# Kernel optimization log

Measured on AMD Instinct MI355X. Metric: run time of the kernel, lower is better.

## Reference

```python
import jax, jax.numpy as jnp
import numpy as np

EPS_NORM = 1e-12
BN_EPS = 1e-5

def rmsnorm(x, gamma):
    # F.normalize(x, dim=-1) * gamma * dim**0.5
    n = jnp.maximum(jnp.linalg.norm(x, axis=-1, keepdims=True), EPS_NORM)
    return x / n * gamma * np.float32(np.sqrt(x.shape[-1]))

def conv1d(x, w, pad):
    # x: (B,C,T), w: (O,I,K)
    return jax.lax.conv_general_dilated(x, w, (1,), [(pad, pad)],
                                        dimension_numbers=('NCH', 'OIH', 'NCH'))

def maxpool3(x):
    # kernel 3, stride 1, pad 1 over last axis
    return jax.lax.reduce_window(x, -jnp.inf, jax.lax.max,
                                 (1, 1, 3), (1, 1, 1), [(0, 0), (0, 0), (1, 1)])

def gelu(x):
    return jax.nn.gelu(x, approximate=False)  # matches torch F.gelu default


def setup_inputs() -> dict:
    key = jax.random.key(0)
    ks = jax.random.split(key, 16)
    B, N, D, E, H, NF = 4, 4096, 512, 4, 1024, 32
    s = 0.02
    inp = {
        'x': jax.random.normal(ks[0], (B, N, D), jnp.float32),
        'left_k': 2048,
        'gamma1': jnp.ones((D,), jnp.float32),
        'gamma2': jnp.ones((D,), jnp.float32),
        'attn_w': jax.random.normal(ks[1], (D, 1), jnp.float32) * s,
        'attn_b': jnp.zeros((1,), jnp.float32),
        'gate_w': jax.random.normal(ks[2], (D, E), jnp.float32) * s,
        'expert_w1': jax.random.normal(ks[3], (E, D, H), jnp.float32) * s,
        'expert_w2': jax.random.normal(ks[4], (E, H, D), jnp.float32) * s,
        'bott_w': jax.random.normal(ks[5], (NF, D, 1), jnp.float32) * s,
        'conv_w39': jax.random.normal(ks[6], (NF, NF, 39), jnp.float32) * s,
        'conv_w19': jax.random.normal(ks[7], (NF, NF, 19), jnp.float32) * s,
        'conv_w9': jax.random.normal(ks[8], (NF, NF, 9), jnp.float32) * s,
        'mp_w': jax.random.normal(ks[9], (NF, D, 1), jnp.float32) * s,
        'bn_g': jnp.ones((NF * 4,), jnp.float32),
        'bn_b': jnp.zeros((NF * 4,), jnp.float32),
        'proj_w': jax.random.normal(ks[10], (NF * 4, D), jnp.float32) * s,
        'proj_b': jnp.zeros((D,), jnp.float32),
    }
    return inp


def reference(x, left_k, gamma1, gamma2, attn_w, attn_b, gate_w,
              expert_w1, expert_w2, bott_w, conv_w39, conv_w19, conv_w9,
              mp_w, bn_g, bn_b, proj_w, proj_b):
    B, N, D = x.shape
    E = gate_w.shape[-1]

    x_n = rmsnorm(x, gamma1)
    scores = jax.nn.sigmoid(x_n @ attn_w + attn_b)            # (B,N,1)
    xs = x_n * scores                                          # (B,N,D)

    # top-k token selection (remain_ratio < 1 path)
    _, top_idx = jax.lax.top_k(scores[..., 0], left_k)         # (B,left_k)
    sorted_idx = jnp.sort(top_idx, axis=1)
    left_x = jnp.take_along_axis(xs, sorted_idx[..., None], axis=1)
    # complement sum via scatter mask (faithful to scatter_/gather/sum)
    sel = jnp.zeros((B, N), x.dtype).at[jnp.arange(B)[:, None], sorted_idx].set(1.0)
    extra = jnp.einsum('bn,bnd->bd', 1.0 - sel, xs)[:, None, :]
    xcat = jnp.concatenate([left_x, extra], axis=1)            # (B,left_k+1,D)

    x_n2 = rmsnorm(xcat, gamma2)

    # dense soft MoE
    gate = jax.nn.softmax(x_n2 @ gate_w, axis=-1)              # (B,T,E)
    h = gelu(jnp.einsum('btd,edh->bteh', x_n2, expert_w1))
    eo = jnp.einsum('bteh,ehd->bted', h, expert_w2)
    moe_out = jnp.einsum('bte,bted->btd', gate, eo)
    moe_loss = E * jnp.sum(jnp.mean(gate, axis=(0, 1)) ** 2)

    # Inception branch (channels-first)
    xc = jnp.transpose(x_n2, (0, 2, 1))                        # (B,D,T)
    xb = conv1d(xc, bott_w, 0)                                 # (B,32,T)
    outs = [conv1d(xb, conv_w39, 19), conv1d(xb, conv_w19, 9),
            conv1d(xb, conv_w9, 4), conv1d(maxpool3(xc), mp_w, 0)]
    cat = jnp.concatenate(outs, axis=1)                        # (B,128,T)
    mu = jnp.mean(cat, axis=(0, 2), keepdims=True)
    var = jnp.var(cat, axis=(0, 2), keepdims=True)
    bn = (cat - mu) / jnp.sqrt(var + BN_EPS) * bn_g[None, :, None] + bn_b[None, :, None]
    incep = gelu(bn)
    incep_out = jnp.transpose(incep, (0, 2, 1)) @ proj_w + proj_b  # (B,T,D)

    out = xcat + moe_out + incep_out
    return gelu(out), moe_loss
```

## Files before the change

kernel.cpp:

```cpp
#include <hip/hip_runtime.h>
#include <hip/hip_bf16.h>
#include <math.h>

#define DEV __device__ __forceinline__

constexpr int B_ = 4, N_ = 4096, D_ = 512, E_ = 4, H_ = 1024, NF_ = 32;
constexpr int KL_ = 2048, T_ = KL_ + 1;
constexpr int TOK_ = B_ * T_;
constexpr int SP_ = 2304;

typedef __bf16 bf16x8 __attribute__((ext_vector_type(8)));
typedef float f32x4 __attribute__((ext_vector_type(4)));

DEV float gelu_f(float x){
  float t = __expf(-1.702f * x);
  return x * __builtin_amdgcn_rcpf(1.0f + t);
}
DEV float bf2f(unsigned short u){ union{unsigned int i; float f;} c; c.i = (unsigned)u << 16; return c.f; }

DEV float wave_sum(float v){
  #pragma unroll
  for (int off = 32; off > 0; off >>= 1) v += __shfl_down(v, off, 64);
  return v;
}

DEV float block_sum256(float v, float* sm){
  v = wave_sum(v);
  int lane = threadIdx.x & 63, wid = threadIdx.x >> 6;
  if (lane == 0) sm[wid] = v;
  __syncthreads();
  if (threadIdx.x == 0) sm[0] = sm[0] + sm[1] + sm[2] + sm[3];
  __syncthreads();
  float r = sm[0];
  __syncthreads();
  return r;
}

__global__ void k_rms_score(const float* __restrict__ x, const float* __restrict__ g,
                            const float* __restrict__ aw, const float* __restrict__ ab,
                            float* __restrict__ scores, float* __restrict__ scale){
  __shared__ float sm[4];
  int row = blockIdx.x; int tid = threadIdx.x;
  const float* xr = x + (size_t)row * D_;
  float v0 = xr[tid], v1 = xr[tid + 256];
  float ss = block_sum256(v0 * v0 + v1 * v1, sm);
  float a  = block_sum256(v0 * g[tid] * aw[tid] + v1 * g[tid + 256] * aw[tid + 256], sm);
  float n = fmaxf(sqrtf(ss), 1e-12f);
  float inv = 22.627416997969522f / n;
  float z = inv * a + ab[0];
  float s = 1.0f / (1.0f + expf(-z));
  if (tid == 0){ scores[row] = s; scale[row] = inv * s; }
}

__global__ void k_select(const float* __restrict__ scores, int* __restrict__ flags){
  __shared__ float s[N_];
  __shared__ int cnts[4][64];
  int b = blockIdx.y; int tid = threadIdx.x;
  int tile = blockIdx.x * 64;
  const float4* src = (const float4*)(scores + (size_t)b * N_);
  for (int j = tid; j < N_ / 4; j += 256) ((float4*)s)[j] = src[j];
  __syncthreads();
  int tok = tid & 63, part = tid >> 6;
  int i = tile + tok;
  float si = s[i];
  int cnt = 0;
  const float4* sp = (const float4*)(s + part * 1024);
  int jb = part * 1024;
  #pragma unroll 4
  for (int j = 0; j < 256; j++){
    float4 v = sp[j];
    int j4 = jb + j * 4;
    cnt += (v.x > si) || (v.x == si && (j4 + 0) < i);
    cnt += (v.y > si) || (v.y == si && (j4 + 1) < i);
    cnt += (v.z > si) || (v.z == si && (j4 + 2) < i);
    cnt += (v.w > si) || (v.w == si && (j4 + 3) < i);
  }
  cnts[part][tok] = cnt;
  __syncthreads();
  if (tid < 64){
    int c = cnts[0][tid] + cnts[1][tid] + cnts[2][tid] + cnts[3][tid];
    flags[(size_t)b * N_ + tile + tid] = (c < KL_) ? 1 : 0;
  }
}

__global__ void k_compact(const int* __restrict__ flags, int* __restrict__ idx){
  __shared__ int wsum[4];
  int b = blockIdx.x; int tid = threadIdx.x;
  const int* fb = flags + (size_t)b * N_;
  int f[16]; int cnt = 0;
  #pragma unroll
  for (int i = 0; i < 16; i++){ f[i] = fb[tid * 16 + i]; cnt += f[i]; }
  int lane = tid & 63, wid = tid >> 6;
  int v = cnt;
  #pragma unroll
  for (int off = 1; off < 64; off <<= 1){
    int t = __shfl_up(v, off, 64);
    if (lane >= off) v += t;
  }
  if (lane == 63) wsum[wid] = v;
  __syncthreads();
  int base = v - cnt;
  for (int w = 0; w < wid; w++) base += wsum[w];
  int* ib = idx + (size_t)b * KL_;
  #pragma unroll
  for (int i = 0; i < 16; i++){
    if (f[i]) ib[base++] = tid * 16 + i;
  }
}

__global__ void k_gather(const float* __restrict__ x, const float* __restrict__ scale,
                         const float* __restrict__ g1, const int* __restrict__ idx,
                         float* __restrict__ xcat){
  size_t i = (size_t)blockIdx.x * 256 + threadIdx.x;
  int d = (int)(i & 511);
  int p = (int)((i >> 9) & (KL_ - 1));
  int b = (int)(i >> 20);
  int tok = idx[(size_t)b * KL_ + p];
  float sc = scale[(size_t)b * N_ + tok];
  xcat[((size_t)b * T_ + p) * D_ + d] = x[((size_t)b * N_ + tok) * D_ + d] * sc * g1[d];
}

__global__ void k_extra1(const float* __restrict__ x, const float* __restrict__ scale,
                         const int* __restrict__ flags, float* __restrict__ part){
  int b = blockIdx.y, blk = blockIdx.x;
  int tid = threadIdx.x;
  const int* fb = flags + (size_t)b * N_ + blk * 64;
  const float* sb = scale + (size_t)b * N_ + blk * 64;
  const float2* xp = (const float2*)(x + ((size_t)b * N_ + blk * 64) * D_) + tid;
  float2 acc = {0.f, 0.f};
  for (int i = 0; i < 64; i++){
    if (!fb[i]){
      float s = sb[i];
      float2 v = xp[(size_t)i * 256];
      acc.x += v.x * s; acc.y += v.y * s;
    }
  }
  float* pr = part + ((size_t)(b * 64 + blk)) * D_;
  pr[tid * 2] = acc.x; pr[tid * 2 + 1] = acc.y;
}

__global__ void k_extra2(const float* __restrict__ part, const float* __restrict__ g1,
                         float* __restrict__ xcat){
  int b = blockIdx.y; int d = blockIdx.x * 256 + threadIdx.x;
  float s = 0.f;
  for (int i = 0; i < 64; i++) s += part[((size_t)(b * 64 + i)) * D_ + d];
  xcat[((size_t)b * T_ + KL_) * D_ + d] = s * g1[d];
}

__global__ void k_rms2gate(const float* __restrict__ xc, const float* __restrict__ g,
                           const float* __restrict__ gw,
                           __hip_bfloat16* __restrict__ xn2b, float* __restrict__ gate){
  __shared__ float sm[4];
  __shared__ float sg[16];
  int row = blockIdx.x; int tid = threadIdx.x;
  const float* xr = xc + (size_t)row * D_;
  float v0 = xr[tid], v1 = xr[tid + 256];
  float ss = block_sum256(v0 * v0 + v1 * v1, sm);
  float n = fmaxf(sqrtf(ss), 1e-12f);
  float inv = 22.627416997969522f / n;
  float xn0 = v0 * inv * g[tid], xn1 = v1 * inv * g[tid + 256];
  __hip_bfloat16* ob = xn2b + (size_t)row * D_;
  ob[tid] = __float2bfloat16(xn0); ob[tid + 256] = __float2bfloat16(xn1);
  const float4* gw4 = (const float4*)gw;
  float4 wa = gw4[tid], wb = gw4[tid + 256];
  float l0 = xn0 * wa.x + xn1 * wb.x, l1 = xn0 * wa.y + xn1 * wb.y;
  float l2 = xn0 * wa.z + xn1 * wb.z, l3 = xn0 * wa.w + xn1 * wb.w;
  l0 = wave_sum(l0); l1 = wave_sum(l1); l2 = wave_sum(l2); l3 = wave_sum(l3);
  int lane = tid & 63, wid = tid >> 6;
  if (lane == 0){ sg[wid*4+0]=l0; sg[wid*4+1]=l1; sg[wid*4+2]=l2; sg[wid*4+3]=l3; }
  __syncthreads();
  if (tid == 0){
    float a0 = sg[0]+sg[4]+sg[8]+sg[12];
    float a1 = sg[1]+sg[5]+sg[9]+sg[13];
    float a2 = sg[2]+sg[6]+sg[10]+sg[14];
    float a3 = sg[3]+sg[7]+sg[11]+sg[15];
    float m = fmaxf(fmaxf(a0, a1), fmaxf(a2, a3));
    float e0 = expf(a0-m), e1 = expf(a1-m), e2 = expf(a2-m), e3 = expf(a3-m);
    float is = 1.f / (e0+e1+e2+e3);
    float* gr = gate + (size_t)row * 4;
    gr[0]=e0*is; gr[1]=e1*is; gr[2]=e2*is; gr[3]=e3*is;
  }
}

__global__ void k_gsumloss(const float* __restrict__ gate, float* __restrict__ o){
  __shared__ float sm[16];
  int tid = threadIdx.x;
  float4 a = {0.f, 0.f, 0.f, 0.f};
  for (int r = tid; r < TOK_; r += 256){
    float4 v = *(const float4*)(gate + (size_t)r * 4);
    a.x += v.x; a.y += v.y; a.z += v.z; a.w += v.w;
  }
  a.x = wave_sum(a.x); a.y = wave_sum(a.y); a.z = wave_sum(a.z); a.w = wave_sum(a.w);
  int lane = tid & 63, wid = tid >> 6;
  if (lane == 0){ sm[wid*4]=a.x; sm[wid*4+1]=a.y; sm[wid*4+2]=a.z; sm[wid*4+3]=a.w; }
  __syncthreads();
  if (tid == 0){
    float l = 0.f;
    #pragma unroll
    for (int e = 0; e < 4; e++){
      float s = sm[e] + sm[4+e] + sm[8+e] + sm[12+e];
      float m = s / (float)TOK_;
      l += m * m;
    }
    o[0] = (float)E_ * l;
  }
}

__global__ void k_trb(const float* __restrict__ in, __hip_bfloat16* __restrict__ out,
                      int R, int C){
  __shared__ float t[32][33];
  int mat = blockIdx.z;
  in  += (size_t)mat * R * C;
  out += (size_t)mat * R * C;
  int c0 = blockIdx.x * 32, r0 = blockIdx.y * 32;
  int j = threadIdx.x & 31, i4 = threadIdx.x >> 5;
  #pragma unroll
  for (int k = 0; k < 4; k++){
    int i = i4 * 4 + k;
    t[i][j] = in[(size_t)(r0 + i) * C + c0 + j];
  }
  __syncthreads();
  #pragma unroll
  for (int k = 0; k < 4; k++){
    int i = i4 * 4 + k;
    out[(size_t)(c0 + i) * R + r0 + j] = __float2bfloat16(t[j][i]);
  }
}

__global__ void k_trb2(const float* __restrict__ in, __hip_bfloat16* __restrict__ out){
  __shared__ float t[32][33];
  int e = blockIdx.z;
  const float* ip = in + (size_t)e * H_ * D_;
  __hip_bfloat16* op = out + (size_t)e * H_;
  int c0 = blockIdx.x * 32, r0 = blockIdx.y * 32;
  int j = threadIdx.x & 31, i4 = threadIdx.x >> 5;
  #pragma unroll
  for (int k = 0; k < 4; k++){
    int i = i4 * 4 + k;
    t[i][j] = ip[(size_t)(r0 + i) * D_ + c0 + j];
  }
  __syncthreads();
  #pragma unroll
  for (int k = 0; k < 4; k++){
    int i = i4 * 4 + k;
    op[(size_t)(c0 + i) * 4096 + r0 + j] = __float2bfloat16(t[j][i]);
  }
}

__global__ void k_wpack(const float* __restrict__ w39, const float* __restrict__ w19,
                        const float* __restrict__ w9, __hip_bfloat16* __restrict__ wcb){
  int i = blockIdx.x * 256 + threadIdx.x;
  if (i >= 73728) return;
  const float* w; int KP, KW, base;
  if (i < 40960){ w = w39; KP = 40; KW = 39; base = 0; }
  else if (i < 61440){ w = w19; KP = 20; KW = 19; base = 40960; }
  else { w = w9; KP = 12; KW = 9; base = 61440; }
  int li = i - base;
  int oc = li / (32 * KP);
  int rem = li % (32 * KP);
  int k = rem >> 5, ic = rem & 31;
  float v = (k < KW) ? w[((size_t)oc * 32 + ic) * KW + k] : 0.f;
  wcb[i] = __float2bfloat16(v);
}

template<int EPI>
__launch_bounds__(512)
__global__ void gemm_bt(const __hip_bfloat16* __restrict__ A,
                        const __hip_bfloat16* __restrict__ Bt,
                        __hip_bfloat16* __restrict__ Cb, size_t zstride,
                        int M, int N, int K, int kloc,
                        const float* __restrict__ gatep){
  __shared__ __align__(16) char smem[2][24576];
  int tid = threadIdx.x;
  unsigned gx = gridDim.x;
  unsigned nwg = gx * gridDim.y;
  unsigned orig = blockIdx.x + gx * blockIdx.y;
  unsigned q = nwg >> 3, r = nwg & 7;
  unsigned xcd = orig & 7, loc = orig >> 3;
  unsigned wg = (xcd < r ? xcd * (q + 1) : r * (q + 1) + (xcd - r) * q) + loc;
  int m0 = (int)(wg / gx) * 256, n0 = (int)(wg % gx) * 128;
  int z = blockIdx.z;
  int koff = z * kloc;
  int ln = tid & 63, wid = tid >> 6;
  int wm = wid >> 1, wn = wid & 1;

  f32x4 acc[4][4] = {};

  auto stage = [&](int buf, int k0){
    #pragma unroll
    for (int c = 0; c < 2; c++){
      int ii = tid + c * 512;
      int rr = ii >> 2, s = ii & 3;
      int gm = m0 + rr; gm = gm < M ? gm : M - 1;
      const __hip_bfloat16* gp = A + (size_t)gm * K + (koff + k0 + ((s ^ (rr & 3)) << 3));
      __builtin_amdgcn_global_load_lds(
          (const __attribute__((address_space(1))) void*)gp,
          (__attribute__((address_space(3))) void*)&smem[buf][ii * 16], 16, 0, 0);
    }
    {
      int ii = tid;
      int rr = ii >> 2, s = ii & 3;
      const __hip_bfloat16* gp = Bt + (size_t)(n0 + rr) * K + (koff + k0 + ((s ^ (rr & 3)) << 3));
      __builtin_amdgcn_global_load_lds(
          (const __attribute__((address_space(1))) void*)gp,
          (__attribute__((address_space(3))) void*)&smem[buf][16384 + ii * 16], 16, 0, 0);
    }
  };

  int nk = kloc >> 5;
  stage(0, 0);
  __syncthreads();
  int slotb = (((ln >> 4) ^ (ln & 3)) << 4);
  for (int t = 0; t < nk; t++){
    int buf = t & 1;
    if (t + 1 < nk) stage(buf ^ 1, (t + 1) << 5);
    bf16x8 af[4], bfr[4];
    #pragma unroll
    for (int m = 0; m < 4; m++){
      int R = wm * 64 + m * 16 + (ln & 15);
      af[m] = *(const bf16x8*)&smem[buf][R * 64 + slotb];
    }
    #pragma unroll
    for (int n = 0; n < 4; n++){
      int R = wn * 64 + n * 16 + (ln & 15);
      bfr[n] = *(const bf16x8*)&smem[buf][16384 + R * 64 + slotb];
    }
    #pragma unroll
    for (int m = 0; m < 4; m++)
      #pragma unroll
      for (int n = 0; n < 4; n++)
        acc[m][n] = __builtin_amdgcn_mfma_f32_16x16x32_bf16(af[m], bfr[n], acc[m][n], 0, 0, 0);
    __syncthreads();
  }

  __hip_bfloat16* Co = Cb + (size_t)z * zstride;
  int e = n0 >> 10;
  #pragma unroll
  for (int m = 0; m < 4; m++){
    int rb = m0 + wm * 64 + m * 16 + ((ln >> 4) << 2);
    float gv[4];
    if (EPI == 1){
      #pragma unroll
      for (int r2 = 0; r2 < 4; r2++)
        gv[r2] = (rb + r2 < M) ? gatep[(size_t)(rb + r2) * 4 + e] : 0.f;
    }
    #pragma unroll
    for (int n = 0; n < 4; n++){
      int col = n0 + wn * 64 + n * 16 + (ln & 15);
      #pragma unroll
      for (int r2 = 0; r2 < 4; r2++){
        int row = rb + r2;
        if (row < M){
          size_t ci = (size_t)row * N + col;
          float v = acc[m][n][r2];
          if (EPI == 0) Co[ci] = __float2bfloat16(v);
          else Co[ci] = __float2bfloat16(gelu_f(v) * gv[r2]);
        }
      }
    }
  }
}

__global__ void k_1x1F(const __hip_bfloat16* __restrict__ xn2b, const float* __restrict__ bw,
                       const float* __restrict__ mw,
                       __hip_bfloat16* __restrict__ xbp, float* __restrict__ cat){
  __shared__ float Xs[32 * 33];
  __shared__ float Ws[32 * 36];
  int type = blockIdx.y;
  const float* w = type == 0 ? bw : mw;
  int tid = threadIdx.x;
  int G0 = blockIdx.x * 32;
  int tok = tid & 31, grp = tid >> 5;
  float acc[4] = {};
  for (int d0 = 0; d0 < D_; d0 += 32){
    {
      int tt = tid >> 3, dc = (tid & 7) * 4;
      int g = G0 + tt;
      float4 v = {0.f, 0.f, 0.f, 0.f};
      if (g < TOK_){
        const __hip_bfloat16* p = xn2b + (size_t)g * D_ + d0 + dc;
        ushort4 rw = *(const ushort4*)p;
        v.x = bf2f(rw.x); v.y = bf2f(rw.y); v.z = bf2f(rw.z); v.w = bf2f(rw.w);
        if (type == 1){
          int t = g % T_;
          if (t > 0){
            ushort4 u = *(const ushort4*)(p - D_);
            v.x = fmaxf(v.x, bf2f(u.x)); v.y = fmaxf(v.y, bf2f(u.y));
            v.z = fmaxf(v.z, bf2f(u.z)); v.w = fmaxf(v.w, bf2f(u.w));
          }
          if (t < T_ - 1){
            ushort4 u = *(const ushort4*)(p + D_);
            v.x = fmaxf(v.x, bf2f(u.x)); v.y = fmaxf(v.y, bf2f(u.y));
            v.z = fmaxf(v.z, bf2f(u.z)); v.w = fmaxf(v.w, bf2f(u.w));
          }
        }
      }
      float* xd = &Xs[tt * 33 + dc];
      xd[0] = v.x; xd[1] = v.y; xd[2] = v.z; xd[3] = v.w;
    }
    for (int j = tid; j < 1024; j += 256){
      int f = j >> 5, d = j & 31;
      Ws[d * 36 + f] = w[(size_t)f * D_ + d0 + d];
    }
    __syncthreads();
    const float* xr = &Xs[tok * 33];
    #pragma unroll 8
    for (int d = 0; d < 32; d++){
      float xv = xr[d];
      const float4* w4 = (const float4*)&Ws[d * 36 + grp * 4];
      float4 a = w4[0];
      acc[0] += xv * a.x; acc[1] += xv * a.y; acc[2] += xv * a.z; acc[3] += xv * a.w;
    }
    __syncthreads();
  }
  int g = G0 + tok;
  if (g < TOK_){
    if (type == 0){
      int bb = g / T_, t = g % T_;
      __hip_bfloat16* op = xbp + ((size_t)(bb * SP_ + 32 + t)) * 32 + grp * 4;
      #pragma unroll
      for (int j = 0; j < 4; j++) op[j] = __float2bfloat16(acc[j]);
    } else {
      float* op = cat + (size_t)g * 128 + 96 + grp * 4;
      #pragma unroll
      for (int j = 0; j < 4; j++) op[j] = acc[j];
    }
  }
}

template<int KP, int PAD, int OFF, int TYPE>
DEV void convm_body(const __hip_bfloat16* __restrict__ xbp,
                    const __hip_bfloat16* __restrict__ wcb,
                    float* __restrict__ cat, char* smem){
  constexpr int R = KP * 32;
  int t0 = blockIdx.x * 128, b = blockIdx.y;
  int tid = threadIdx.x;
  for (int j = tid; j < 768; j += 256){
    int r = j >> 2, c = j & 3;
    int rg = b * SP_ + 32 + t0 - PAD + r;
    const __hip_bfloat16* gp = xbp + (size_t)rg * 32 + ((c ^ (r & 3)) << 3);
    __builtin_amdgcn_global_load_lds(
        (const __attribute__((address_space(1))) void*)gp,
        (__attribute__((address_space(3))) void*)(smem + j * 16), 16, 0, 0);
  }
  __syncthreads();
  int ln = tid & 63, wid = tid >> 6;
  int lr = ln & 15, lg = ln >> 4;
  int tb = wid * 32;
  const __hip_bfloat16* wt = wcb + OFF;
  const __hip_bfloat16* bp0 = wt + (size_t)lr * R + lg * 8;
  const __hip_bfloat16* bp1 = wt + (size_t)(16 + lr) * R + lg * 8;
  f32x4 acc[2][2] = {};
  bf16x8 bc0 = *(const bf16x8*)bp0;
  bf16x8 bc1 = *(const bf16x8*)bp1;
  #pragma unroll 4
  for (int s = 0; s < KP; s++){
    bf16x8 bn0 = bc0, bn1 = bc1;
    if (s + 1 < KP){
      bn0 = *(const bf16x8*)(bp0 + (s + 1) * 32);
      bn1 = *(const bf16x8*)(bp1 + (s + 1) * 32);
    }
    int ra0 = tb + lr + s;
    int ra1 = tb + 16 + lr + s;
    bf16x8 a0 = *(const bf16x8*)(smem + ra0 * 64 + ((lg ^ (ra0 & 3)) << 4));
    bf16x8 a1 = *(const bf16x8*)(smem + ra1 * 64 + ((lg ^ (ra1 & 3)) << 4));
    acc[0][0] = __builtin_amdgcn_mfma_f32_16x16x32_bf16(a0, bc0, acc[0][0], 0, 0, 0);
    acc[0][1] = __builtin_amdgcn_mfma_f32_16x16x32_bf16(a0, bc1, acc[0][1], 0, 0, 0);
    acc[1][0] = __builtin_amdgcn_mfma_f32_16x16x32_bf16(a1, bc0, acc[1][0], 0, 0, 0);
    acc[1][1] = __builtin_amdgcn_mfma_f32_16x16x32_bf16(a1, bc1, acc[1][1], 0, 0, 0);
    bc0 = bn0; bc1 = bn1;
  }
  #pragma unroll
  for (int m = 0; m < 2; m++){
    int rb = tb + m * 16 + ((ln >> 4) << 2);
    #pragma unroll
    for (int n = 0; n < 2; n++){
      int oc = n * 16 + lr;
      #pragma unroll
      for (int j2 = 0; j2 < 4; j2++){
        int tp = t0 + rb + j2;
        if (tp < T_)
          cat[((size_t)b * T_ + tp) * 128 + TYPE * 32 + oc] = acc[m][n][j2];
      }
    }
  }
}

__global__ __launch_bounds__(256)
void k_convM(const __hip_bfloat16* __restrict__ xbp,
             const __hip_bfloat16* __restrict__ wcb, float* __restrict__ cat){
  __shared__ __align__(16) char smem[192 * 64];
  if (blockIdx.z == 0)      convm_body<40, 19, 0,     0>(xbp, wcb, cat, smem);
  else if (blockIdx.z == 1) convm_body<20, 9,  40960, 1>(xbp, wcb, cat, smem);
  else                      convm_body<12, 4,  61440, 2>(xbp, wcb, cat, smem);
}

__global__ void k_bnstat(const float* __restrict__ cat, float* __restrict__ stats){
  __shared__ float sm[512];
  int tid = threadIdx.x;
  float s = 0.f, q = 0.f;
  for (int rp = blockIdx.x; rp < TOK_ / 2; rp += gridDim.x){
    float v = cat[(size_t)rp * 256 + tid];
    s += v; q += v * v;
  }
  sm[tid] = s; sm[256 + tid] = q;
  __syncthreads();
  if (tid < 128){
    atomicAdd(&stats[tid], sm[tid] + sm[tid + 128]);
    atomicAdd(&stats[128 + tid], sm[256 + tid] + sm[256 + tid + 128]);
  }
}

__global__ void k_bnact(const float* __restrict__ cat, __hip_bfloat16* __restrict__ catb,
                        const float* __restrict__ stats,
                        const float* __restrict__ g, const float* __restrict__ b){
  int i = blockIdx.x * 256 + threadIdx.x;
  int c = i & 127;
  float mu = stats[c] * (1.f / TOK_);
  float var = stats[128 + c] * (1.f / TOK_) - mu * mu;
  float v = cat[i];
  v = (v - mu) * rsqrtf(var + 1e-5f) * g[c] + b[c];
  catb[i] = __float2bfloat16(gelu_f(v));
}

__global__ void k_final(const float* __restrict__ xcat, const __hip_bfloat16* __restrict__ moeb,
                        size_t zs, const __hip_bfloat16* __restrict__ ioutb,
                        const float* __restrict__ pb, float* __restrict__ out){
  size_t i = ((size_t)blockIdx.x * 256 + threadIdx.x) * 2;
  int d = (int)(i & 511);
  float2 xc = *(const float2*)&xcat[i];
  float s0 = xc.x, s1 = xc.y;
  #pragma unroll
  for (int z = 0; z < 4; z++){
    unsigned u = *(const unsigned*)&moeb[(size_t)z * zs + i];
    s0 += bf2f((unsigned short)(u & 0xffff));
    s1 += bf2f((unsigned short)(u >> 16));
  }
  unsigned v = *(const unsigned*)&ioutb[i];
  s0 += bf2f((unsigned short)(v & 0xffff));
  s1 += bf2f((unsigned short)(v >> 16));
  s0 += pb[d]; s1 += pb[d + 1];
  out[i] = gelu_f(s0); out[i + 1] = gelu_f(s1);
}

extern "C" void kernel_launch(void* const* d_in, const int* in_sizes, int n_in,
                              void* d_out, int out_size, void* d_ws, size_t ws_size,
                              hipStream_t stream){
  const float* x      = (const float*)d_in[0];
  const float* gamma1 = (const float*)d_in[2];
  const float* gamma2 = (const float*)d_in[3];
  const float* attn_w = (const float*)d_in[4];
  const float* attn_b = (const float*)d_in[5];
  const float* gate_w = (const float*)d_in[6];
  const float* ew1    = (const float*)d_in[7];
  const float* ew2    = (const float*)d_in[8];
  const float* bott_w = (const float*)d_in[9];
  const float* w39    = (const float*)d_in[10];
  const float* w19    = (const float*)d_in[11];
  const float* w9     = (const float*)d_in[12];
  const float* mp_w   = (const float*)d_in[13];
  const float* bn_g   = (const float*)d_in[14];
  const float* bn_b   = (const float*)d_in[15];
  const float* proj_w = (const float*)d_in[16];
  const float* proj_b = (const float*)d_in[17];
  float* out = (float*)d_out;

  float* ws = (float*)d_ws;
  size_t off = 0;
  auto alloc = [&](size_t n){ size_t o = off; off += (n + 63) & ~(size_t)63; return o; };
  size_t f_hb   = alloc((size_t)TOK_ * 4096 / 2);
  size_t f_sc   = alloc(B_ * N_);
  size_t f_sca  = alloc(B_ * N_);
  size_t f_fl   = alloc(B_ * N_);
  size_t f_idx  = alloc(B_ * KL_);
  size_t f_xcat = alloc((size_t)TOK_ * D_);
  size_t f_moeb = alloc((size_t)4 * TOK_ * D_ / 2 + 64);
  size_t f_gate = alloc(TOK_ * E_);
  size_t f_st   = alloc(256);
  size_t f_xbp  = alloc((size_t)B_ * SP_ * 32 / 2);
  size_t f_cat  = alloc((size_t)TOK_ * 128);
  size_t f_wb   = alloc((size_t)(E_ * D_ * H_) + (size_t)TOK_ * D_ / 2 + 64);
  size_t f_part = alloc((size_t)B_ * 64 * D_);
  size_t f_wcb  = alloc(73728 / 2 + 64);
  size_t f_pjb  = alloc(512 * 128 / 2 + 64);
  (void)ws_size; (void)in_sizes; (void)n_in; (void)out_size;

  float* sc   = ws + f_sc;
  float* sca  = ws + f_sca;
  int*   fl   = (int*)(ws + f_fl);
  int*   idx  = (int*)(ws + f_idx);
  float* xcat = ws + f_xcat;
  float* gate = ws + f_gate;
  float* stats= ws + f_st;
  float* cat  = ws + f_cat;
  float* part = ws + f_part;
  __hip_bfloat16* moeb  = (__hip_bfloat16*)(ws + f_moeb);
  __hip_bfloat16* xbp   = (__hip_bfloat16*)(ws + f_xbp);
  __hip_bfloat16* wcb   = (__hip_bfloat16*)(ws + f_wcb);
  __hip_bfloat16* projb = (__hip_bfloat16*)(ws + f_pjb);
  __hip_bfloat16* hbuf  = (__hip_bfloat16*)(ws + f_hb);
  __hip_bfloat16* ioutb = (__hip_bfloat16*)(ws + f_hb);
  __hip_bfloat16* catb  = (__hip_bfloat16*)(ws + f_hb + 4196416);
  __hip_bfloat16* w1b  = (__hip_bfloat16*)(ws + f_wb);
  __hip_bfloat16* w2b  = w1b + (size_t)E_ * D_ * H_;
  __hip_bfloat16* xn2b = w2b + (size_t)E_ * D_ * H_;

  hipMemsetAsync(stats, 0, 256 * sizeof(float), stream);
  hipMemsetAsync(xbp, 0, (size_t)B_ * SP_ * 32 * sizeof(__hip_bfloat16), stream);

  k_trb<<<dim3(H_/32, D_/32, E_), 256, 0, stream>>>(ew1, w1b, D_, H_);
  k_trb2<<<dim3(D_/32, H_/32, E_), 256, 0, stream>>>(ew2, w2b);
  k_trb<<<dim3(D_/32, 128/32, 1), 256, 0, stream>>>(proj_w, projb, 128, D_);
  k_wpack<<<288, 256, 0, stream>>>(w39, w19, w9, wcb);

  k_rms_score<<<B_ * N_, 256, 0, stream>>>(x, gamma1, attn_w, attn_b, sc, sca);
  k_select<<<dim3(N_ / 64, B_), 256, 0, stream>>>(sc, fl);
  k_compact<<<B_, 256, 0, stream>>>(fl, idx);
  k_gather<<<(B_ * KL_ * D_) / 256, 256, 0, stream>>>(x, sca, gamma1, idx, xcat);
  k_extra1<<<dim3(64, B_), 256, 0, stream>>>(x, sca, fl, part);
  k_extra2<<<dim3(2, B_), 256, 0, stream>>>(part, gamma1, xcat);
  k_rms2gate<<<TOK_, 256, 0, stream>>>(xcat, gamma2, gate_w, xn2b, gate);
  k_gsumloss<<<1, 256, 0, stream>>>(gate, out + (size_t)TOK_ * D_);

  int mt = (TOK_ + 255) / 256;
  size_t zs = (size_t)TOK_ * D_;
  gemm_bt<1><<<dim3(4096/128, mt), 512, 0, stream>>>(
      xn2b, w1b, hbuf, 0, TOK_, 4096, D_, D_, gate);
  gemm_bt<0><<<dim3(D_/128, mt, 4), 512, 0, stream>>>(
      hbuf, w2b, moeb, zs, TOK_, D_, 4096, 1024, nullptr);

  int t32 = (TOK_ + 31) / 32;
  k_1x1F<<<dim3(t32, 2), 256, 0, stream>>>(xn2b, bott_w, mp_w, xbp, cat);
  k_convM<<<dim3(17, 4, 3), 256, 0, stream>>>(xbp, wcb, cat);
  k_bnstat<<<256, 256, 0, stream>>>(cat, stats);
  k_bnact<<<(TOK_ * 128) / 256, 256, 0, stream>>>(cat, catb, stats, bn_g, bn_b);
  gemm_bt<0><<<dim3(D_/128, mt), 512, 0, stream>>>(
      catb, projb, ioutb, 0, TOK_, D_, 128, 128, nullptr);
  k_final<<<((size_t)TOK_ * D_) / 512, 256, 0, stream>>>(xcat, moeb, zs, ioutb, proj_b, out);
}
```

Baseline: 326.5 us.

## Use triple-buffered 128x128 GEMM tiles with 256 threads and single barrier

The bf16 GEMM moves from a 256x128 tile with 512 threads and double buffering to a 128x128 tile with 256 threads. It adds a three-stage LDS ring that prefetches two K-steps ahead. Each iteration uses one explicit vmcnt wait plus barrier instead of two __syncthreads. MFMA issue is wrapped in s_setprio so math waves get priority over loads. The aim is better hiding of global-to-LDS latency and more workgroups for the small-M GEMMs, at the cost of less A/B reuse per tile and more reliance on a hand-counted vmcnt value.

```diff
diff --git a/kernel.cpp b/kernel.cpp
--- a/kernel.cpp
+++ b/kernel.cpp
@@ -264,13 +264,13 @@
 }
 
 template<int EPI>
-__launch_bounds__(512)
+__launch_bounds__(256)
 __global__ void gemm_bt(const __hip_bfloat16* __restrict__ A,
                         const __hip_bfloat16* __restrict__ Bt,
                         __hip_bfloat16* __restrict__ Cb, size_t zstride,
                         int M, int N, int K, int kloc,
                         const float* __restrict__ gatep){
-  __shared__ __align__(16) char smem[2][24576];
+  __shared__ __align__(16) char smem[3][16384];
   int tid = threadIdx.x;
   unsigned gx = gridDim.x;
   unsigned nwg = gx * gridDim.y;
@@ -278,7 +278,7 @@
   unsigned q = nwg >> 3, r = nwg & 7;
   unsigned xcd = orig & 7, loc = orig >> 3;
   unsigned wg = (xcd < r ? xcd * (q + 1) : r * (q + 1) + (xcd - r) * q) + loc;
-  int m0 = (int)(wg / gx) * 256, n0 = (int)(wg % gx) * 128;
+  int m0 = (int)(wg / gx) * 128, n0 = (int)(wg % gx) * 128;
   int z = blockIdx.z;
   int koff = z * kloc;
   int ln = tid & 63, wid = tid >> 6;
@@ -286,51 +286,62 @@
 
   f32x4 acc[4][4] = {};
 
-  auto stage = [&](int buf, int k0){
+  auto stage = [&](char* buf, int k0){
     #pragma unroll
     for (int c = 0; c < 2; c++){
-      int ii = tid + c * 512;
+      int ii = tid + c * 256;
       int rr = ii >> 2, s = ii & 3;
       int gm = m0 + rr; gm = gm < M ? gm : M - 1;
       const __hip_bfloat16* gp = A + (size_t)gm * K + (koff + k0 + ((s ^ (rr & 3)) << 3));
       __builtin_amdgcn_global_load_lds(
           (const __attribute__((address_space(1))) void*)gp,
-          (__attribute__((address_space(3))) void*)&smem[buf][ii * 16], 16, 0, 0);
-    }
-    {
-      int ii = tid;
+          (__attribute__((address_space(3))) void*)(buf + ii * 16), 16, 0, 0);
+    }
+    #pragma unroll
+    for (int c = 0; c < 2; c++){
+      int ii = tid + c * 256;
       int rr = ii >> 2, s = ii & 3;
       const __hip_bfloat16* gp = Bt + (size_t)(n0 + rr) * K + (koff + k0 + ((s ^ (rr & 3)) << 3));
       __builtin_amdgcn_global_load_lds(
           (const __attribute__((address_space(1))) void*)gp,
-          (__attribute__((address_space(3))) void*)&smem[buf][16384 + ii * 16], 16, 0, 0);
+          (__attribute__((address_space(3))) void*)(buf + 8192 + ii * 16), 16, 0, 0);
     }
   };
 
   int nk = kloc >> 5;
-  stage(0, 0);
-  __syncthreads();
+  stage(smem[0], 0);
+  stage(smem[1], 32);
   int slotb = (((ln >> 4) ^ (ln & 3)) << 4);
+  int cur = 0;
   for (int t = 0; t < nk; t++){
-    int buf = t & 1;
-    if (t + 1 < nk) stage(buf ^ 1, (t + 1) << 5);
+    if (t + 1 < nk) asm volatile("s_waitcnt vmcnt(4)" ::: "memory");
+    else            asm volatile("s_waitcnt vmcnt(0)" ::: "memory");
+    __builtin_amdgcn_s_barrier();
+    __builtin_amdgcn_sched_barrier(0);
+    if (t + 2 < nk){
+      int nxt = cur + 2; if (nxt >= 3) nxt -= 3;
+      stage(smem[nxt], (t + 2) << 5);
+    }
+    char* buf = smem[cur];
     bf16x8 af[4], bfr[4];
     #pragma unroll
     for (int m = 0; m < 4; m++){
       int R = wm * 64 + m * 16 + (ln & 15);
-      af[m] = *(const bf16x8*)&smem[buf][R * 64 + slotb];
+      af[m] = *(const bf16x8*)(buf + R * 64 + slotb);
     }
     #pragma unroll
     for (int n = 0; n < 4; n++){
       int R = wn * 64 + n * 16 + (ln & 15);
-      bfr[n] = *(const bf16x8*)&smem[buf][16384 + R * 64 + slotb];
-    }
+      bfr[n] = *(const bf16x8*)(buf + 8192 + R * 64 + slotb);
+    }
+    __builtin_amdgcn_s_setprio(1);
     #pragma unroll
     for (int m = 0; m < 4; m++)
       #pragma unroll
       for (int n = 0; n < 4; n++)
         acc[m][n] = __builtin_amdgcn_mfma_f32_16x16x32_bf16(af[m], bfr[n], acc[m][n], 0, 0, 0);
-    __syncthreads();
+    __builtin_amdgcn_s_setprio(0);
+    cur = (cur == 2) ? 0 : cur + 1;
   }
 
   __hip_bfloat16* Co = Cb + (size_t)z * zstride;
@@ -622,11 +633,11 @@
   k_rms2gate<<<TOK_, 256, 0, stream>>>(xcat, gamma2, gate_w, xn2b, gate);
   k_gsumloss<<<1, 256, 0, stream>>>(gate, out + (size_t)TOK_ * D_);
 
-  int mt = (TOK_ + 255) / 256;
+  int mt = (TOK_ + 127) / 128;
   size_t zs = (size_t)TOK_ * D_;
-  gemm_bt<1><<<dim3(4096/128, mt), 512, 0, stream>>>(
+  gemm_bt<1><<<dim3(4096/128, mt), 256, 0, stream>>>(
       xn2b, w1b, hbuf, 0, TOK_, 4096, D_, D_, gate);
-  gemm_bt<0><<<dim3(D_/128, mt, 4), 512, 0, stream>>>(
+  gemm_bt<0><<<dim3(D_/128, mt, 4), 256, 0, stream>>>(
       hbuf, w2b, moeb, zs, TOK_, D_, 4096, 1024, nullptr);
 
   int t32 = (TOK_ + 31) / 32;
@@ -634,7 +645,7 @@
   k_convM<<<dim3(17, 4, 3), 256, 0, stream>>>(xbp, wcb, cat);
   k_bnstat<<<256, 256, 0, stream>>>(cat, stats);
   k_bnact<<<(TOK_ * 128) / 256, 256, 0, stream>>>(cat, catb, stats, bn_g, bn_b);
-  gemm_bt<0><<<dim3(D_/128, mt), 512, 0, stream>>>(
+  gemm_bt<0><<<dim3(D_/128, mt), 256, 0, stream>>>(
       catb, projb, ioutb, 0, TOK_, D_, 128, 128, nullptr);
   k_final<<<((size_t)TOK_ * D_) / 512, 256, 0, stream>>>(xcat, moeb, zs, ioutb, proj_b, out);
 }
```

New measurement: 325.9 us. Within noise of the previous version (-0.2%).

## Permute MoE output columns so GEMM epilogue writes packed 8-byte bf16 stores

Applied to the files above, without the earlier changes.

The expert_w2 transpose now writes a permuted column order within each 64-wide group, so every lane's four MFMA output columns land next to each other in memory. The GEMM epilogue then packs four bf16 values into one uint2 store instead of four scattered 2-byte stores. The final kernel undoes the permutation when it reads xcat and the bias and when it writes the output. This trades fewer, wider epilogue stores for scattered 4-byte accesses in k_final. The layout must stay consistent across the three kernels.

```diff
diff --git a/kernel.cpp b/kernel.cpp
--- a/kernel.cpp
+++ b/kernel.cpp
@@ -17,6 +17,11 @@
   return x * __builtin_amdgcn_rcpf(1.0f + t);
 }
 DEV float bf2f(unsigned short u){ union{unsigned int i; float f;} c; c.i = (unsigned)u << 16; return c.f; }
+DEV unsigned pack2(float a, float b){
+  __hip_bfloat16 ha = __float2bfloat16(a), hb = __float2bfloat16(b);
+  unsigned short ua = *(unsigned short*)&ha, ub = *(unsigned short*)&hb;
+  return (unsigned)ua | ((unsigned)ub << 16);
+}
 
 DEV float wave_sum(float v){
   #pragma unroll
@@ -243,7 +248,9 @@
   #pragma unroll
   for (int k = 0; k < 4; k++){
     int i = i4 * 4 + k;
-    op[(size_t)(c0 + i) * 4096 + r0 + j] = __float2bfloat16(t[j][i]);
+    int v = r0 + j;
+    int pv = (v & ~63) | ((v & 15) << 2) | ((v >> 4) & 3);
+    op[(size_t)(c0 + i) * 4096 + pv] = __float2bfloat16(t[j][i]);
   }
 }
 
@@ -335,6 +342,7 @@
 
   __hip_bfloat16* Co = Cb + (size_t)z * zstride;
   int e = n0 >> 10;
+  int lr = ln & 15;
   #pragma unroll
   for (int m = 0; m < 4; m++){
     int rb = m0 + wm * 64 + m * 16 + ((ln >> 4) << 2);
@@ -345,17 +353,18 @@
         gv[r2] = (rb + r2 < M) ? gatep[(size_t)(rb + r2) * 4 + e] : 0.f;
     }
     #pragma unroll
-    for (int n = 0; n < 4; n++){
-      int col = n0 + wn * 64 + n * 16 + (ln & 15);
-      #pragma unroll
-      for (int r2 = 0; r2 < 4; r2++){
-        int row = rb + r2;
-        if (row < M){
-          size_t ci = (size_t)row * N + col;
-          float v = acc[m][n][r2];
-          if (EPI == 0) Co[ci] = __float2bfloat16(v);
-          else Co[ci] = __float2bfloat16(gelu_f(v) * gv[r2]);
+    for (int r2 = 0; r2 < 4; r2++){
+      int row = rb + r2;
+      if (row < M){
+        float v0 = acc[m][0][r2], v1 = acc[m][1][r2];
+        float v2 = acc[m][2][r2], v3 = acc[m][3][r2];
+        if (EPI == 1){
+          v0 = gelu_f(v0) * gv[r2]; v1 = gelu_f(v1) * gv[r2];
+          v2 = gelu_f(v2) * gv[r2]; v3 = gelu_f(v3) * gv[r2];
         }
+        uint2 pk; pk.x = pack2(v0, v1); pk.y = pack2(v2, v3);
+        size_t ci = (size_t)row * N + (n0 + wn * 64 + 4 * lr);
+        *(uint2*)&Co[ci] = pk;
       }
     }
   }
@@ -527,9 +536,9 @@
                         size_t zs, const __hip_bfloat16* __restrict__ ioutb,
                         const float* __restrict__ pb, float* __restrict__ out){
   size_t i = ((size_t)blockIdx.x * 256 + threadIdx.x) * 2;
-  int d = (int)(i & 511);
-  float2 xc = *(const float2*)&xcat[i];
-  float s0 = xc.x, s1 = xc.y;
+  int p = (int)(i & 511);
+  size_t rowbase = i - p;
+  float s0 = 0.f, s1 = 0.f;
   #pragma unroll
   for (int z = 0; z < 4; z++){
     unsigned u = *(const unsigned*)&moeb[(size_t)z * zs + i];
@@ -539,8 +548,13 @@
   unsigned v = *(const unsigned*)&ioutb[i];
   s0 += bf2f((unsigned short)(v & 0xffff));
   s1 += bf2f((unsigned short)(v >> 16));
-  s0 += pb[d]; s1 += pb[d + 1];
-  out[i] = gelu_f(s0); out[i + 1] = gelu_f(s1);
+  int d0 = (p & ~63) | ((p & 3) << 4) | ((p >> 2) & 15);
+  int p1 = p + 1;
+  int d1 = (p1 & ~63) | ((p1 & 3) << 4) | ((p1 >> 2) & 15);
+  s0 += xcat[rowbase + d0] + pb[d0];
+  s1 += xcat[rowbase + d1] + pb[d1];
+  out[rowbase + d0] = gelu_f(s0);
+  out[rowbase + d1] = gelu_f(s1);
 }
 
 extern "C" void kernel_launch(void* const* d_in, const int* in_sizes, int n_in,
```

Result: faster. 313.7 us (-3.9%).
